# Optimization experiments

Measured on AMD Instinct MI355X. Metric: run time of the kernel, lower is better.

Reference implementation:

```python
import jax, jax.numpy as jnp
import numpy as np

Q = 1          # hard-coded in the original forward
LAM = 1e-3     # ridge regularizer of the ELM-AE least-squares solve


def setup_inputs() -> dict:
    key = jax.random.key(0)
    k1, k2 = jax.random.split(key)
    B, Z, H, W = 64, 512, 32, 32
    x = jax.random.normal(k1, (B, Z, H, W), dtype=jnp.float32)
    # fixed random ELM hidden-layer weights (Q x z); the repo generates these
    # with a deterministic LCG, here plain gaussian random
    Wh = jax.random.normal(k2, (Q, Z), dtype=jnp.float32)
    return {"x": x, "W": Wh}


def reference(x, W):
    # x: [B, Z, h, w]  -> per-sample feature matrix X: [Z, N] with N = h*w pixels
    B, Z, h, w = x.shape
    X = x.reshape(B, Z, h * w)                      # [B, Z, N]
    # ELM-AE: random hidden activations over pixels
    Hh = jax.nn.sigmoid(jnp.einsum('qz,bzn->bqn', W, X))   # [B, Q, N]
    G = jnp.einsum('bqn,bpn->bqp', Hh, Hh) + LAM * jnp.eye(Q, dtype=x.dtype)  # [B, Q, Q]
    XHt = jnp.einsum('bzn,bqn->bzq', X, Hh)         # [B, Z, Q]
    # solve G^T Beta^T = XHt^T  (G symmetric)
    Beta = jnp.swapaxes(jnp.linalg.solve(G, jnp.swapaxes(XHt, 1, 2)), 1, 2)  # [B, Z, Q]
    # pooled features flattened to (B, Q*Z, 1) as in the original
    out = Beta.reshape(B, Q * Z, 1)
    return out
```

## Files before the change

kernel.cpp:

```cpp
#include <hip/hip_runtime.h>
#include <hip/hip_bf16.h>

#define B_ 64
#define Z_ 512
#define N_ 1024
#define LAM 1e-3f
#define NQ 32
#define NC 32
#define TH 512
#define WS_XH (B_ * NQ * Z_)

__global__ __launch_bounds__(TH, 8) void elm_k1(
    const float* __restrict__ x, const float* __restrict__ Wh,
    float* __restrict__ pxh, float* __restrict__ gws) {
  __shared__ float part[8][NC];
  __shared__ float h_lds[NC];

  const int t   = threadIdx.x;
  const int bid = blockIdx.x;
  const int b   = bid >> 5;
  const int nq  = bid & 31;
  const int jg  = t & 7;
  const int zr  = t >> 3;
  const int wv  = t >> 6;
  const int ln  = t & 63;

  const float* xp = x + (size_t)b * (Z_ * N_) + (size_t)zr * N_ + (nq * NC + jg * 4);

  float4 v[8];
#pragma unroll
  for (int k = 0; k < 8; ++k)
    v[k] = *reinterpret_cast<const float4*>(xp + (size_t)(64 * k) * N_);

  float w[8];
#pragma unroll
  for (int k = 0; k < 8; ++k) w[k] = Wh[zr + 64 * k];

  float sp[4];
#pragma unroll
  for (int i = 0; i < 4; ++i) {
    float s = 0.f;
#pragma unroll
    for (int k = 0; k < 8; ++k) s += w[k] * reinterpret_cast<const float*>(&v[k])[i];
    s += __shfl_xor(s, 8);
    s += __shfl_xor(s, 16);
    s += __shfl_xor(s, 32);
    sp[i] = s;
  }
  if (ln < 8) {
#pragma unroll
    for (int i = 0; i < 4; ++i) part[wv][ln * 4 + i] = sp[i];
  }
  __syncthreads();

  if (t < NC) {
    float s = 0.f;
#pragma unroll
    for (int w8 = 0; w8 < 8; ++w8) s += part[w8][t];
    const float h = 1.f / (1.f + __expf(-s));
    h_lds[t] = h;
    float q = h * h;
    q += __shfl_xor(q, 1);
    q += __shfl_xor(q, 2);
    q += __shfl_xor(q, 4);
    q += __shfl_xor(q, 8);
    q += __shfl_xor(q, 16);
    if (t == 0) gws[bid] = q;
  }
  __syncthreads();

  float acc[8] = {0.f, 0.f, 0.f, 0.f, 0.f, 0.f, 0.f, 0.f};
#pragma unroll
  for (int i = 0; i < 4; ++i) {
    const float h = h_lds[jg * 4 + i];
#pragma unroll
    for (int k = 0; k < 8; ++k) acc[k] += h * reinterpret_cast<const float*>(&v[k])[i];
  }
#pragma unroll
  for (int k = 0; k < 8; ++k) {
    float a = acc[k];
    a += __shfl_xor(a, 1);
    a += __shfl_xor(a, 2);
    a += __shfl_xor(a, 4);
    if (jg == 0) pxh[(size_t)bid * Z_ + zr + 64 * k] = a;
  }
}

__global__ __launch_bounds__(Z_) void elm_k2(
    const float* __restrict__ pxh, const float* __restrict__ gws,
    float* __restrict__ out) {
  const int b = blockIdx.x;
  const int t = threadIdx.x;
  __shared__ float ginv;
  if (t < 32) {
    float g = gws[b * NQ + t];
    g += __shfl_xor(g, 1);
    g += __shfl_xor(g, 2);
    g += __shfl_xor(g, 4);
    g += __shfl_xor(g, 8);
    g += __shfl_xor(g, 16);
    if (t == 0) ginv = 1.f / (g + LAM);
  }
  __syncthreads();
  float s = 0.f;
#pragma unroll
  for (int nq = 0; nq < NQ; ++nq) s += pxh[((size_t)b * NQ + nq) * Z_ + t];
  out[b * Z_ + t] = s * ginv;
}

extern "C" void kernel_launch(void* const* d_in, const int* in_sizes, int n_in,
                              void* d_out, int out_size, void* d_ws, size_t ws_size,
                              hipStream_t stream) {
  const float* x  = (const float*)d_in[0];
  const float* Wh = (const float*)d_in[1];
  float* out = (float*)d_out;
  float* pxh = (float*)d_ws;
  float* gws = (float*)d_ws + WS_XH;

  elm_k1<<<dim3(B_ * NQ), dim3(TH), 0, stream>>>(x, Wh, pxh, gws);
  elm_k2<<<dim3(B_), dim3(Z_), 0, stream>>>(pxh, gws, out);
}
```

Before: 30.89 us.

## Process four pixel slices per block with double-buffered register loads

Each block now handles 128 pixels as four 32-pixel slices, ping-ponging two register buffers so the next slice's global loads are in flight while the current one is reduced. This cuts the grid from 2048 to 512 blocks, and the partials written to the workspace and summed in the second kernel shrink by 4x. The second kernel's cross-lane reduction and shared-memory broadcast are replaced by a direct loop over 8 partials, and the barriers are hand-written. In exchange, register pressure rises, the occupancy hint drops from 8 to 4, and fewer blocks are left to hide memory latency.

```diff
diff --git a/kernel.cpp b/kernel.cpp
--- a/kernel.cpp
+++ b/kernel.cpp
@@ -5,85 +5,112 @@
 #define Z_ 512
 #define N_ 1024
 #define LAM 1e-3f
-#define NQ 32
+#define PB 8
+#define NSL 4
 #define NC 32
 #define TH 512
-#define WS_XH (B_ * NQ * Z_)
+#define WS_XH (B_ * PB * Z_)
+#define WS_G  (B_ * PB)
 
-__global__ __launch_bounds__(TH, 8) void elm_k1(
+__device__ __forceinline__ void lds_barrier() {
+  asm volatile("s_waitcnt lgkmcnt(0)" ::: "memory");
+  __builtin_amdgcn_sched_barrier(0);
+  __builtin_amdgcn_s_barrier();
+  __builtin_amdgcn_sched_barrier(0);
+}
+
+__global__ __launch_bounds__(TH, 4) void elm_k1(
     const float* __restrict__ x, const float* __restrict__ Wh,
     float* __restrict__ pxh, float* __restrict__ gws) {
   __shared__ float part[8][NC];
   __shared__ float h_lds[NC];
 
   const int t   = threadIdx.x;
-  const int bid = blockIdx.x;
-  const int b   = bid >> 5;
-  const int nq  = bid & 31;
+  const int blk = blockIdx.x;
+  const int b   = blk >> 3;
+  const int p   = blk & 7;
   const int jg  = t & 7;
   const int zr  = t >> 3;
   const int wv  = t >> 6;
   const int ln  = t & 63;
 
-  const float* xp = x + (size_t)b * (Z_ * N_) + (size_t)zr * N_ + (nq * NC + jg * 4);
-
-  float4 v[8];
-#pragma unroll
-  for (int k = 0; k < 8; ++k)
-    v[k] = *reinterpret_cast<const float4*>(xp + (size_t)(64 * k) * N_);
+  const float* xp = x + (size_t)b * (Z_ * N_) + (size_t)zr * N_ + (p * 128 + jg * 4);
 
   float w[8];
 #pragma unroll
   for (int k = 0; k < 8; ++k) w[k] = Wh[zr + 64 * k];
 
-  float sp[4];
-#pragma unroll
-  for (int i = 0; i < 4; ++i) {
-    float s = 0.f;
-#pragma unroll
-    for (int k = 0; k < 8; ++k) s += w[k] * reinterpret_cast<const float*>(&v[k])[i];
-    s += __shfl_xor(s, 8);
-    s += __shfl_xor(s, 16);
-    s += __shfl_xor(s, 32);
-    sp[i] = s;
-  }
-  if (ln < 8) {
-#pragma unroll
-    for (int i = 0; i < 4; ++i) part[wv][ln * 4 + i] = sp[i];
-  }
-  __syncthreads();
+  float acc[8] = {0.f, 0.f, 0.f, 0.f, 0.f, 0.f, 0.f, 0.f};
+  float gacc = 0.f;
+  float4 va[8], vb[8];
 
-  if (t < NC) {
-    float s = 0.f;
-#pragma unroll
-    for (int w8 = 0; w8 < 8; ++w8) s += part[w8][t];
-    const float h = 1.f / (1.f + __expf(-s));
-    h_lds[t] = h;
-    float q = h * h;
-    q += __shfl_xor(q, 1);
-    q += __shfl_xor(q, 2);
-    q += __shfl_xor(q, 4);
-    q += __shfl_xor(q, 8);
-    q += __shfl_xor(q, 16);
-    if (t == 0) gws[bid] = q;
-  }
-  __syncthreads();
+#define LOADS(V, S)                                                          \
+  _Pragma("unroll") for (int k = 0; k < 8; ++k)                              \
+      V[k] = *reinterpret_cast<const float4*>(xp + (size_t)(64 * k) * N_ + (S) * NC);
 
-  float acc[8] = {0.f, 0.f, 0.f, 0.f, 0.f, 0.f, 0.f, 0.f};
-#pragma unroll
-  for (int i = 0; i < 4; ++i) {
-    const float h = h_lds[jg * 4 + i];
-#pragma unroll
-    for (int k = 0; k < 8; ++k) acc[k] += h * reinterpret_cast<const float*>(&v[k])[i];
-  }
+#define PROC(V)                                                              \
+  do {                                                                       \
+    float sp[4];                                                             \
+    _Pragma("unroll") for (int i = 0; i < 4; ++i) {                          \
+      float s_ = 0.f;                                                        \
+      _Pragma("unroll") for (int k = 0; k < 8; ++k)                          \
+          s_ += w[k] * reinterpret_cast<const float*>(&V[k])[i];             \
+      s_ += __shfl_xor(s_, 8);                                               \
+      s_ += __shfl_xor(s_, 16);                                              \
+      s_ += __shfl_xor(s_, 32);                                              \
+      sp[i] = s_;                                                            \
+    }                                                                        \
+    if (ln < 8) {                                                            \
+      _Pragma("unroll") for (int i = 0; i < 4; ++i)                          \
+          part[wv][ln * 4 + i] = sp[i];                                      \
+    }                                                                        \
+    lds_barrier();                                                           \
+    {                                                                        \
+      float q_ = 0.f;                                                        \
+      if (t < NC) {                                                          \
+        float s_ = 0.f;                                                      \
+        _Pragma("unroll") for (int w8 = 0; w8 < 8; ++w8)                     \
+            s_ += part[w8][t];                                               \
+        const float h_ = 1.f / (1.f + __expf(-s_));                          \
+        h_lds[t] = h_;                                                       \
+        q_ = h_ * h_;                                                        \
+        q_ += __shfl_xor(q_, 1);                                             \
+        q_ += __shfl_xor(q_, 2);                                             \
+        q_ += __shfl_xor(q_, 4);                                             \
+        q_ += __shfl_xor(q_, 8);                                             \
+        q_ += __shfl_xor(q_, 16);                                            \
+      }                                                                      \
+      if (t == 0) gacc += q_;                                                \
+    }                                                                        \
+    lds_barrier();                                                           \
+    _Pragma("unroll") for (int i = 0; i < 4; ++i) {                          \
+      const float hh = h_lds[jg * 4 + i];                                    \
+      _Pragma("unroll") for (int k = 0; k < 8; ++k)                          \
+          acc[k] += hh * reinterpret_cast<const float*>(&V[k])[i];           \
+    }                                                                        \
+  } while (0)
+
+  LOADS(va, 0);
+  LOADS(vb, 1);
+  PROC(va);
+  LOADS(va, 2);
+  PROC(vb);
+  LOADS(vb, 3);
+  PROC(va);
+  PROC(vb);
+
+#undef LOADS
+#undef PROC
+
 #pragma unroll
   for (int k = 0; k < 8; ++k) {
     float a = acc[k];
     a += __shfl_xor(a, 1);
     a += __shfl_xor(a, 2);
     a += __shfl_xor(a, 4);
-    if (jg == 0) pxh[(size_t)bid * Z_ + zr + 64 * k] = a;
+    if (jg == 0) pxh[(size_t)blk * Z_ + zr + 64 * k] = a;
   }
+  if (t == 0) gws[blk] = gacc;
 }
 
 __global__ __launch_bounds__(Z_) void elm_k2(
@@ -91,21 +118,13 @@
     float* __restrict__ out) {
   const int b = blockIdx.x;
   const int t = threadIdx.x;
-  __shared__ float ginv;
-  if (t < 32) {
-    float g = gws[b * NQ + t];
-    g += __shfl_xor(g, 1);
-    g += __shfl_xor(g, 2);
-    g += __shfl_xor(g, 4);
-    g += __shfl_xor(g, 8);
-    g += __shfl_xor(g, 16);
-    if (t == 0) ginv = 1.f / (g + LAM);
-  }
-  __syncthreads();
+  float g = LAM;
+#pragma unroll
+  for (int p = 0; p < PB; ++p) g += gws[b * PB + p];
   float s = 0.f;
 #pragma unroll
-  for (int nq = 0; nq < NQ; ++nq) s += pxh[((size_t)b * NQ + nq) * Z_ + t];
-  out[b * Z_ + t] = s * ginv;
+  for (int p = 0; p < PB; ++p) s += pxh[((size_t)b * PB + p) * Z_ + t];
+  out[b * Z_ + t] = s / g;
 }
 
 extern "C" void kernel_launch(void* const* d_in, const int* in_sizes, int n_in,
@@ -117,6 +136,6 @@
   float* pxh = (float*)d_ws;
   float* gws = (float*)d_ws + WS_XH;
 
-  elm_k1<<<dim3(B_ * NQ), dim3(TH), 0, stream>>>(x, Wh, pxh, gws);
+  elm_k1<<<dim3(B_ * PB), dim3(TH), 0, stream>>>(x, Wh, pxh, gws);
   elm_k2<<<dim3(B_), dim3(Z_), 0, stream>>>(pxh, gws, out);
 }
```

Result: slower. 45.08 us (+46.0%).
